# Kernel optimization log

Hardware: AMD Instinct MI355X
Metric: run time of the kernel (lower is better)

## Reference

```python
import jax, jax.numpy as jnp
import numpy as np

N, E, F = 50000, 1_600_000, 128
EPS = 1e-5
DATASET_NUM = 1.0


def _glorot(k, shape):
    lim = jnp.sqrt(6.0 / (shape[0] + shape[1]))
    return jax.random.uniform(k, shape, jnp.float32, -lim, lim)


def setup_inputs() -> dict:
    key = jax.random.key(0)
    ks = jax.random.split(key, 24)
    inp = {
        "x": jax.random.normal(ks[0], (N, F), jnp.float32),
        "noise": jax.random.normal(ks[1], (N, F), jnp.float32),
        "edge_index": jax.random.randint(ks[2], (2, E), 0, N, jnp.int64),
        # ChebConv K=2 weights: W0 (T_0 = x term), W1 (T_1 = L_hat x term)
        "W1_0": _glorot(ks[3], (F, 64)),  "W1_1": _glorot(ks[4], (F, 64)),  "b1": jnp.zeros((64,), jnp.float32),
        "g1": jnp.ones((64,), jnp.float32), "be1": jnp.zeros((64,), jnp.float32),
        "W2_0": _glorot(ks[5], (64, 16)), "W2_1": _glorot(ks[6], (64, 16)), "b2": jnp.zeros((16,), jnp.float32),
        "W3_0": _glorot(ks[7], (16, 64)), "W3_1": _glorot(ks[8], (16, 64)), "b3": jnp.zeros((64,), jnp.float32),
        "g3": jnp.ones((64,), jnp.float32), "be3": jnp.zeros((64,), jnp.float32),
        "W4_0": _glorot(ks[9], (64, F)),  "W4_1": _glorot(ks[10], (64, F)), "b4": jnp.zeros((F,), jnp.float32),
    }
    return inp


def reference(x, noise, edge_index, W1_0, W1_1, b1, g1, be1,
              W2_0, W2_1, b2, W3_0, W3_1, b3, g3, be3, W4_0, W4_1, b4):
    src, dst = edge_index[0], edge_index[1]
    n = x.shape[0]

    # train-mode noise injection: x + dataset_num * randn * x.mean()
    x = x + DATASET_NUM * noise * jnp.mean(x)

    # symmetric normalization; with lambda_max=2 the scaled Laplacian is -A_norm
    deg = jax.ops.segment_sum(jnp.ones_like(src, dtype=x.dtype), dst, num_segments=n)
    dinv = jnp.where(deg > 0, jax.lax.rsqrt(jnp.maximum(deg, 1.0)), 0.0)
    w_e = dinv[src] * dinv[dst]  # [E]

    def cheb(h, W0, W1, b):
        # T_0 = h ; T_1 = L_hat h = -A_norm h  (K=2 ChebConv)
        tx1 = -jax.ops.segment_sum(w_e[:, None] * h[src], dst, num_segments=n)
        return h @ W0 + tx1 @ W1 + b

    def bn(h, g, be):
        mu = jnp.mean(h, axis=0)
        var = jnp.mean((h - mu) ** 2, axis=0)
        return g * (h - mu) * jax.lax.rsqrt(var + EPS) + be

    h1 = jax.nn.relu(bn(cheb(x, W1_0, W1_1, b1), g1, be1))
    h2 = cheb(h1, W2_0, W2_1, b2)
    h3 = jax.nn.relu(bn(cheb(h2, W3_0, W3_1, b3), g3, be3))
    return cheb(h3, W4_0, W4_1, b4)
```

## Files before the change

### kernel.cpp

```cpp
#include <hip/hip_runtime.h>

#define NNODES 50000
#define NEDGES 1600000
#define FEAT   128
#define EPSV   1e-5f

typedef _Float16 h8 __attribute__((ext_vector_type(8)));
typedef _Float16 h4 __attribute__((ext_vector_type(4)));

__device__ __forceinline__ float4 f4fma(float s, float4 w, float4 a) {
  a.x = fmaf(s, w.x, a.x); a.y = fmaf(s, w.y, a.y);
  a.z = fmaf(s, w.z, a.z); a.w = fmaf(s, w.w, a.w);
  return a;
}

__global__ __launch_bounds__(256) void sum_kernel(const float* __restrict__ x,
                                                  float* __restrict__ out, int n4) {
  const float4* x4 = (const float4*)x;
  float s = 0.f;
  for (int i = blockIdx.x * blockDim.x + threadIdx.x; i < n4; i += gridDim.x * blockDim.x) {
    float4 v = x4[i];
    s += v.x + v.y + v.z + v.w;
  }
  for (int off = 32; off > 0; off >>= 1) s += __shfl_down(s, off);
  __shared__ float ls[4];
  int wid = threadIdx.x >> 6;
  if ((threadIdx.x & 63) == 0) ls[wid] = s;
  __syncthreads();
  if (threadIdx.x == 0) atomicAdd(out, ls[0] + ls[1] + ls[2] + ls[3]);
}

__global__ __launch_bounds__(256) void degree_kernel(const int* __restrict__ ei,
                                                     int* __restrict__ degi, int ne) {
  int e = blockIdx.x * blockDim.x + threadIdx.x;
  if (e < ne) atomicAdd(&degi[ei[NEDGES + e]], 1);
}

__global__ __launch_bounds__(256) void dinv_kernel(const int* __restrict__ degi,
                                                   float* __restrict__ dinv, int n) {
  int i = blockIdx.x * blockDim.x + threadIdx.x;
  if (i < n) dinv[i] = (degi[i] > 0) ? rsqrtf((float)degi[i]) : 0.f;
}

__global__ __launch_bounds__(1024) void scan1_kernel(const int* __restrict__ cnt,
                                                     int* __restrict__ exc,
                                                     int* __restrict__ bsum, int n) {
  __shared__ int s[1024];
  int tid = threadIdx.x;
  int i = blockIdx.x * 1024 + tid;
  int v = (i < n) ? cnt[i] : 0;
  int val = v;
  s[tid] = v;
  __syncthreads();
  for (int off = 1; off < 1024; off <<= 1) {
    int t = (tid >= off) ? s[tid - off] : 0;
    __syncthreads();
    val += t;
    s[tid] = val;
    __syncthreads();
  }
  if (i < n) exc[i] = val - v;
  if (tid == 1023) bsum[blockIdx.x] = val;
}

__global__ __launch_bounds__(256) void scan2_kernel(int* __restrict__ bsum, int nb) {
  __shared__ int s[256];
  int tid = threadIdx.x;
  int v = (tid < nb) ? bsum[tid] : 0;
  int val = v;
  s[tid] = v;
  __syncthreads();
  for (int off = 1; off < 256; off <<= 1) {
    int t = (tid >= off) ? s[tid - off] : 0;
    __syncthreads();
    val += t;
    s[tid] = val;
    __syncthreads();
  }
  if (tid < nb) bsum[tid] = val - v;
}

__global__ __launch_bounds__(256) void scan3_kernel(int* __restrict__ row_ptr,
                                                    const int* __restrict__ bsum,
                                                    int* __restrict__ cursor, int n) {
  int i = blockIdx.x * blockDim.x + threadIdx.x;
  if (i < n) {
    int v = row_ptr[i] + bsum[i >> 10];
    row_ptr[i] = v;
    cursor[i] = v;
  } else if (i == n) {
    row_ptr[n] = NEDGES;
  }
}

__global__ __launch_bounds__(256) void csr_fill_kernel(const int* __restrict__ ei,
                                                       const float* __restrict__ dinv,
                                                       int* __restrict__ cursor,
                                                       int2* __restrict__ ep, int ne) {
  int e = blockIdx.x * blockDim.x + threadIdx.x;
  if (e >= ne) return;
  int s = ei[e];
  int d = ei[NEDGES + e];
  float w = dinv[s] * dinv[d];
  int pos = atomicAdd(&cursor[d], 1);
  ep[pos] = make_int2(s, __float_as_int(w));
}

template <int F, bool ADD, bool STATS, bool BNIN, bool OUTH>
__global__ __launch_bounds__(256) void spmm_kernel(
    const int* __restrict__ row_ptr, const int2* __restrict__ ep,
    const _Float16* __restrict__ gsrc, const float* __restrict__ addL,
    const float* __restrict__ bias,
    const float* __restrict__ stats_in, const float* __restrict__ gin,
    const float* __restrict__ bein, float* __restrict__ stats_out,
    void* __restrict__ outv, int n) {
  constexpr int LPE = F / 8;
  constexpr int EPC = 64 / LPE;
  constexpr int LG  = (LPE == 2) ? 1 : 3;
  __shared__ float sst[STATS ? 2 * F : 1];
  const int tid = threadIdx.x;
  if (STATS) {
    if (tid < 2 * F) sst[tid] = 0.f;
    __syncthreads();
  }
  const int lane = tid & 63;
  const int wv = tid >> 6;
  const int sub = lane & (LPE - 1);
  const int g = lane >> LG;
  const int f0 = sub * 8;
  float scl[8], sht[8];
  if (BNIN) {
    const float inv_n = 1.0f / (float)n;
#pragma unroll
    for (int j = 0; j < 8; ++j) {
      int f = f0 + j;
      float mu = stats_in[f] * inv_n;
      float var = stats_in[F + f] * inv_n - mu * mu;
      float s = gin[f] * rsqrtf(var + EPSV);
      scl[j] = s;
      sht[j] = bein[f] - mu * s;
    }
  }
  for (int node = blockIdx.x * 4 + wv; node < n; node += gridDim.x * 4) {
    float acc[8] = {};
    const int beg = row_ptr[node], end = row_ptr[node + 1];
    int e = beg + g;
    while (e < end) {
      int2 s0 = ep[e];
      bool p1 = (e + EPC) < end;
      int2 s1 = ep[p1 ? e + EPC : e];
      float w0 = __int_as_float(s0.y);
      float w1 = p1 ? __int_as_float(s1.y) : 0.f;
      h8 r0 = *(const h8*)(gsrc + (size_t)s0.x * F + f0);
      h8 r1 = *(const h8*)(gsrc + (size_t)s1.x * F + f0);
#pragma unroll
      for (int j = 0; j < 8; ++j) {
        float v0 = (float)r0[j], v1 = (float)r1[j];
        if (BNIN) {
          v0 = fmaxf(fmaf(v0, scl[j], sht[j]), 0.f);
          v1 = fmaxf(fmaf(v1, scl[j], sht[j]), 0.f);
        }
        acc[j] = fmaf(w0, v0, acc[j]);
        acc[j] = fmaf(w1, v1, acc[j]);
      }
      e += 2 * EPC;
    }
#pragma unroll
    for (int m = LPE; m < 64; m <<= 1) {
#pragma unroll
      for (int j = 0; j < 8; ++j) acc[j] += __shfl_xor(acc[j], m);
    }
    if (lane < LPE) {
      float o[8];
      if (ADD) {
        float4 a0 = *(const float4*)&addL[(size_t)node * F + f0];
        float4 a1 = *(const float4*)&addL[(size_t)node * F + f0 + 4];
        float4 b0 = *(const float4*)&bias[f0];
        float4 b1 = *(const float4*)&bias[f0 + 4];
        o[0] = a0.x + b0.x - acc[0]; o[1] = a0.y + b0.y - acc[1];
        o[2] = a0.z + b0.z - acc[2]; o[3] = a0.w + b0.w - acc[3];
        o[4] = a1.x + b1.x - acc[4]; o[5] = a1.y + b1.y - acc[5];
        o[6] = a1.z + b1.z - acc[6]; o[7] = a1.w + b1.w - acc[7];
      } else {
#pragma unroll
        for (int j = 0; j < 8; ++j) o[j] = -acc[j];
      }
      if (OUTH) {
        h8 ho;
#pragma unroll
        for (int j = 0; j < 8; ++j) ho[j] = (_Float16)o[j];
        *(h8*)((_Float16*)outv + (size_t)node * F + f0) = ho;
      } else {
        float* op = (float*)outv + (size_t)node * F + f0;
        *(float4*)op = make_float4(o[0], o[1], o[2], o[3]);
        *(float4*)(op + 4) = make_float4(o[4], o[5], o[6], o[7]);
      }
      if (STATS) {
#pragma unroll
        for (int j = 0; j < 8; ++j) {
          atomicAdd(&sst[f0 + j], o[j]);
          atomicAdd(&sst[F + f0 + j], o[j] * o[j]);
        }
      }
    }
  }
  if (STATS) {
    __syncthreads();
    if (tid < 2 * F) atomicAdd(&stats_out[tid], sst[tid]);
  }
}

template <int K, int NB, bool ROWCAT, bool BIAS, bool BNIN, bool STATS, bool NOISE,
          bool A1H, int OMODE>
__global__ __launch_bounds__(256) void gemm_kernel(
    const void* __restrict__ A1, const float* __restrict__ A2,
    const float* __restrict__ W0, const float* __restrict__ W1,
    const float* __restrict__ bias, int col0, int wnt, int ostride, int ocol0,
    const float* __restrict__ noise, const float* __restrict__ sumv,
    const float* __restrict__ stats_in, const float* __restrict__ gin,
    const float* __restrict__ bein, float* __restrict__ stats_out,
    void* __restrict__ outv, void* __restrict__ out2, int n) {
  constexpr int TC  = NB / 4;
  constexpr int RG  = 256 / TC;
  constexpr int RPT = 4;
  constexpr int RPB = RG * RPT;
  constexpr int AP  = K + 4;
  constexpr int KB  = ROWCAT ? K / 2 : K;
  __shared__ float wl[K * NB];
  __shared__ float al[RPB * AP];
  __shared__ float sarr[BNIN ? KB : 1];
  __shared__ float tarr[BNIN ? KB : 1];
  __shared__ float sst[STATS ? 2 * NB : 1];
  const int tid = threadIdx.x;
  if (STATS && tid < 2 * NB) sst[tid] = 0.f;
  if (BNIN) {
    const float inv_n = 1.0f / (float)n;
    for (int f = tid; f < KB; f += 256) {
      float mu = stats_in[f] * inv_n;
      float var = stats_in[KB + f] * inv_n - mu * mu;
      float s = gin[f] * rsqrtf(var + EPSV);
      sarr[f] = s;
      tarr[f] = bein[f] - mu * s;
    }
  }
  float mean = 0.f;
  if (NOISE) mean = sumv[0] * (1.0f / (float)(NNODES * FEAT));

  for (int i = tid; i < K * NB; i += 256) {
    int k = i / NB, j = i - k * NB;
    int jg = col0 + j;
    float v;
    if (ROWCAT) v = (k < K / 2) ? W0[k * wnt + jg] : W1[(k - K / 2) * wnt + jg];
    else        v = (jg < wnt / 2) ? W0[k * (wnt / 2) + jg] : W1[k * (wnt / 2) + (jg - wnt / 2)];
    wl[i] = v;
  }
  __syncthreads();

  const int row0 = blockIdx.x * RPB;
  for (int i = tid; i < RPB * K; i += 256) {
    int r = i / K, k = i - r * K;
    int gr = row0 + r;
    float v = 0.f;
    if (gr < n) {
      if (ROWCAT) {
        if (k < K / 2) {
          v = A1H ? (float)((const _Float16*)A1)[(size_t)gr * (K / 2) + k]
                  : ((const float*)A1)[(size_t)gr * (K / 2) + k];
          if (BNIN) v = fmaxf(fmaf(v, sarr[k], tarr[k]), 0.f);
        } else {
          v = A2[(size_t)gr * (K / 2) + (k - K / 2)];
        }
      } else {
        v = A1H ? (float)((const _Float16*)A1)[(size_t)gr * K + k]
                : ((const float*)A1)[(size_t)gr * K + k];
        if (BNIN) v = fmaxf(fmaf(v, sarr[k], tarr[k]), 0.f);
        if (NOISE) v = fmaf(noise[(size_t)gr * K + k], mean, v);
      }
    }
    al[r * AP + k] = v;
  }
  __syncthreads();

  const int jt = (tid % TC) * 4;
  const int rbase = (tid / TC) * RPT;
  float4 acc[RPT];
#pragma unroll
  for (int rr = 0; rr < RPT; ++rr) acc[rr] = make_float4(0.f, 0.f, 0.f, 0.f);
  const float4* wl4 = (const float4*)wl;
  const int jt4 = jt >> 2;
#pragma unroll 4
  for (int k0 = 0; k0 < K; k0 += 4) {
    float4 w0 = wl4[(k0 + 0) * TC + jt4];
    float4 w1 = wl4[(k0 + 1) * TC + jt4];
    float4 w2 = wl4[(k0 + 2) * TC + jt4];
    float4 w3 = wl4[(k0 + 3) * TC + jt4];
#pragma unroll
    for (int rr = 0; rr < RPT; ++rr) {
      float4 a = *(const float4*)&al[(rbase + rr) * AP + k0];
      acc[rr] = f4fma(a.x, w0, acc[rr]);
      acc[rr] = f4fma(a.y, w1, acc[rr]);
      acc[rr] = f4fma(a.z, w2, acc[rr]);
      acc[rr] = f4fma(a.w, w3, acc[rr]);
    }
  }
  float4 b4 = make_float4(0.f, 0.f, 0.f, 0.f);
  if (BIAS) b4 = *(const float4*)&bias[col0 + jt];
  float sl[4] = {}, ql[4] = {};
#pragma unroll
  for (int rr = 0; rr < RPT; ++rr) {
    int gr = row0 + rbase + rr;
    if (gr < n) {
      float4 o;
      o.x = acc[rr].x + b4.x; o.y = acc[rr].y + b4.y;
      o.z = acc[rr].z + b4.z; o.w = acc[rr].w + b4.w;
      if (OMODE == 0) {
        *(float4*)((float*)outv + (size_t)gr * ostride + ocol0 + jt) = o;
      } else if (OMODE == 1) {
        h4 ho; ho[0] = (_Float16)o.x; ho[1] = (_Float16)o.y;
        ho[2] = (_Float16)o.z; ho[3] = (_Float16)o.w;
        *(h4*)((_Float16*)outv + (size_t)gr * ostride + ocol0 + jt) = ho;
      } else {
        if (jt < 16) {
          *(float4*)((float*)outv + (size_t)gr * 16 + jt) = o;
        } else {
          h4 ho; ho[0] = (_Float16)o.x; ho[1] = (_Float16)o.y;
          ho[2] = (_Float16)o.z; ho[3] = (_Float16)o.w;
          *(h4*)((_Float16*)out2 + (size_t)gr * 16 + (jt - 16)) = ho;
        }
      }
      if (STATS) {
        sl[0] += o.x; ql[0] += o.x * o.x; sl[1] += o.y; ql[1] += o.y * o.y;
        sl[2] += o.z; ql[2] += o.z * o.z; sl[3] += o.w; ql[3] += o.w * o.w;
      }
    }
  }
  if (STATS) {
#pragma unroll
    for (int j = 0; j < 4; ++j) {
      atomicAdd(&sst[jt + j], sl[j]);
      atomicAdd(&sst[NB + jt + j], ql[j]);
    }
    __syncthreads();
    if (tid < 2 * NB) atomicAdd(&stats_out[tid], sst[tid]);
  }
}

extern "C" void kernel_launch(void* const* d_in, const int* in_sizes, int n_in,
                              void* d_out, int out_size, void* d_ws, size_t ws_size,
                              hipStream_t stream) {
  const float* x     = (const float*)d_in[0];
  const float* noise = (const float*)d_in[1];
  const int*   ei    = (const int*)d_in[2];
  const float* W1_0 = (const float*)d_in[3];
  const float* W1_1 = (const float*)d_in[4];
  const float* b1   = (const float*)d_in[5];
  const float* g1   = (const float*)d_in[6];
  const float* be1  = (const float*)d_in[7];
  const float* W2_0 = (const float*)d_in[8];
  const float* W2_1 = (const float*)d_in[9];
  const float* b2   = (const float*)d_in[10];
  const float* W3_0 = (const float*)d_in[11];
  const float* W3_1 = (const float*)d_in[12];
  const float* b3   = (const float*)d_in[13];
  const float* g3   = (const float*)d_in[14];
  const float* be3  = (const float*)d_in[15];
  const float* W4_0 = (const float*)d_in[16];
  const float* W4_1 = (const float*)d_in[17];
  const float* b4   = (const float*)d_in[18];
  float* out = (float*)d_out;

  char* p = (char*)d_ws;
  size_t off = 0;
  auto alloc = [&](size_t b) -> void* {
    void* r = p + off;
    off += (b + 255) & ~(size_t)255;
    return r;
  };
  float* s_sum  = (float*)alloc(4);
  float* stats0 = (float*)alloc(2 * 64 * 4);
  float* stats1 = (float*)alloc(2 * 64 * 4);
  int*   degi   = (int*)alloc(sizeof(int) * NNODES);
  size_t zero_bytes = off;
  float*     dinv    = (float*)alloc(sizeof(float) * NNODES);
  int*       row_ptr = (int*)alloc(sizeof(int) * (NNODES + 1));
  int*       bsum    = (int*)alloc(256 * sizeof(int));
  int*       cursor  = (int*)alloc(sizeof(int) * NNODES);
  int2*      ep      = (int2*)alloc(8ULL * NEDGES);
  float*     zzL     = (float*)alloc(4ULL * NNODES * 64);
  _Float16*  zzRh    = (_Float16*)alloc(2ULL * NNODES * 64);
  float*     h1      = (float*)alloc(4ULL * NNODES * 64);
  _Float16*  zz2Rh   = (_Float16*)alloc(2ULL * NNODES * 16);
  _Float16*  h2      = (_Float16*)alloc(2ULL * NNODES * 16);
  _Float16*  h3h     = (_Float16*)alloc(2ULL * NNODES * 64);
  float*     agg4    = zzL;

  float* zz2L = out;
  float* agg3 = out + (size_t)NNODES * 16;

  hipMemsetAsync(d_ws, 0, zero_bytes, stream);

  int n4 = NNODES * FEAT / 4;
  sum_kernel<<<2048, 256, 0, stream>>>(x, s_sum, n4);
  degree_kernel<<<(NEDGES + 255) / 256, 256, 0, stream>>>(ei, degi, NEDGES);
  dinv_kernel<<<(NNODES + 255) / 256, 256, 0, stream>>>(degi, dinv, NNODES);
  scan1_kernel<<<(NNODES + 1023) / 1024, 1024, 0, stream>>>(degi, row_ptr, bsum, NNODES);
  scan2_kernel<<<1, 256, 0, stream>>>(bsum, (NNODES + 1023) / 1024);
  scan3_kernel<<<(NNODES + 256) / 256, 256, 0, stream>>>(row_ptr, bsum, cursor, NNODES);
  csr_fill_kernel<<<(NEDGES + 255) / 256, 256, 0, stream>>>(ei, dinv, cursor, ep, NEDGES);

  gemm_kernel<128, 64, false, false, false, false, true, false, 0>
      <<<(NNODES + 63) / 64, 256, 0, stream>>>(
      x, nullptr, W1_0, W1_1, nullptr, 0, 128, 64, 0,
      noise, s_sum, nullptr, nullptr, nullptr, nullptr, zzL, nullptr, NNODES);
  gemm_kernel<128, 64, false, false, false, false, true, false, 1>
      <<<(NNODES + 63) / 64, 256, 0, stream>>>(
      x, nullptr, W1_0, W1_1, nullptr, 64, 128, 64, 0,
      noise, s_sum, nullptr, nullptr, nullptr, nullptr, zzRh, nullptr, NNODES);
  spmm_kernel<64, true, true, false, false><<<2048, 256, 0, stream>>>(
      row_ptr, ep, zzRh, zzL, b1, nullptr, nullptr, nullptr, stats0, h1, NNODES);

  gemm_kernel<64, 32, false, false, true, false, false, false, 2>
      <<<(NNODES + 127) / 128, 256, 0, stream>>>(
      h1, nullptr, W2_0, W2_1, nullptr, 0, 32, 16, 0,
      nullptr, nullptr, stats0, g1, be1, nullptr, zz2L, zz2Rh, NNODES);
  spmm_kernel<16, true, false, false, true><<<2048, 256, 0, stream>>>(
      row_ptr, ep, zz2Rh, zz2L, b2, nullptr, nullptr, nullptr, nullptr, h2, NNODES);

  spmm_kernel<16, false, false, false, false><<<2048, 256, 0, stream>>>(
      row_ptr, ep, h2, nullptr, nullptr, nullptr, nullptr, nullptr, nullptr, agg3, NNODES);
  gemm_kernel<32, 64, true, true, false, true, false, true, 1>
      <<<(NNODES + 63) / 64, 256, 0, stream>>>(
      h2, agg3, W3_0, W3_1, b3, 0, 64, 64, 0,
      nullptr, nullptr, nullptr, nullptr, nullptr, stats1, h3h, nullptr, NNODES);

  spmm_kernel<64, false, false, true, false><<<2048, 256, 0, stream>>>(
      row_ptr, ep, h3h, nullptr, nullptr, stats1, g3, be3, nullptr, agg4, NNODES);
  gemm_kernel<128, 64, true, true, true, false, false, true, 0>
      <<<(NNODES + 63) / 64, 256, 0, stream>>>(
      h3h, agg4, W4_0, W4_1, b4, 0, 128, 128, 0,
      nullptr, nullptr, stats1, g3, be3, nullptr, out, nullptr, NNODES);
  gemm_kernel<128, 64, true, true, true, false, false, true, 0>
      <<<(NNODES + 63) / 64, 256, 0, stream>>>(
      h3h, agg4, W4_0, W4_1, b4, 64, 128, 128, 64,
      nullptr, nullptr, stats1, g3, be3, nullptr, out, nullptr, NNODES);
}
```

Before: 683.5 us.

## Build CSR via two-pass bucketed binning instead of scattered atomic fill

Replaces the single scattered csr_fill pass with a two-stage binning. The first pass groups each 4096-edge chunk by 512-node destination bucket in shared memory and writes packed (src, local dst) words contiguously into a staging buffer that reuses the output array. The second pass handles one bucket per block, so the cursor atomics and ep writes land in a narrow, cache-friendly region. This adds an extra kernel and a staging round trip, and the 16-bit source packing relies on the node count being below 65536.

```diff
diff --git a/kernel.cpp b/kernel.cpp
--- a/kernel.cpp
+++ b/kernel.cpp
@@ -4,6 +4,7 @@
 #define NEDGES 1600000
 #define FEAT   128
 #define EPSV   1e-5f
+#define NBUCK  ((NNODES + 511) / 512)
 
 typedef _Float16 h8 __attribute__((ext_vector_type(8)));
 typedef _Float16 h4 __attribute__((ext_vector_type(4)));
@@ -82,28 +83,88 @@
 
 __global__ __launch_bounds__(256) void scan3_kernel(int* __restrict__ row_ptr,
                                                     const int* __restrict__ bsum,
-                                                    int* __restrict__ cursor, int n) {
+                                                    int* __restrict__ cursor,
+                                                    int* __restrict__ gcur, int n) {
   int i = blockIdx.x * blockDim.x + threadIdx.x;
   if (i < n) {
     int v = row_ptr[i] + bsum[i >> 10];
     row_ptr[i] = v;
     cursor[i] = v;
+    if ((i & 511) == 0) gcur[i >> 9] = v;
   } else if (i == n) {
     row_ptr[n] = NEDGES;
   }
 }
 
-__global__ __launch_bounds__(256) void csr_fill_kernel(const int* __restrict__ ei,
-                                                       const float* __restrict__ dinv,
-                                                       int* __restrict__ cursor,
-                                                       int2* __restrict__ ep, int ne) {
-  int e = blockIdx.x * blockDim.x + threadIdx.x;
-  if (e >= ne) return;
-  int s = ei[e];
-  int d = ei[NEDGES + e];
-  float w = dinv[s] * dinv[d];
-  int pos = atomicAdd(&cursor[d], 1);
-  ep[pos] = make_int2(s, __float_as_int(w));
+__global__ __launch_bounds__(256) void binA_kernel(const int* __restrict__ ei,
+                                                   int* __restrict__ gcur,
+                                                   unsigned int* __restrict__ gstage,
+                                                   int ne) {
+  __shared__ int hist[NBUCK];
+  __shared__ int prefix[NBUCK + 1];
+  __shared__ int offs[NBUCK];
+  __shared__ int gbase[NBUCK];
+  __shared__ unsigned int stag[4096];
+  const int tid = threadIdx.x;
+  const int c0 = blockIdx.x * 4096;
+  for (int b = tid; b < NBUCK; b += 256) hist[b] = 0;
+  __syncthreads();
+  for (int i = tid; i < 4096; i += 256) {
+    int e = c0 + i;
+    if (e < ne) atomicAdd(&hist[ei[NEDGES + e] >> 9], 1);
+  }
+  __syncthreads();
+  if (tid == 0) {
+    int s = 0;
+    for (int b = 0; b < NBUCK; ++b) { prefix[b] = s; s += hist[b]; }
+    prefix[NBUCK] = s;
+  }
+  __syncthreads();
+  if (tid < NBUCK) {
+    offs[tid] = prefix[tid];
+    gbase[tid] = atomicAdd(&gcur[tid], hist[tid]);
+  }
+  __syncthreads();
+  for (int i = tid; i < 4096; i += 256) {
+    int e = c0 + i;
+    if (e < ne) {
+      int s = ei[e];
+      int d = ei[NEDGES + e];
+      int b = d >> 9;
+      int p = atomicAdd(&offs[b], 1);
+      stag[p] = (unsigned int)s | ((unsigned int)(d & 511) << 16);
+    }
+  }
+  __syncthreads();
+  const int total = prefix[NBUCK];
+  for (int j = tid; j < total; j += 256) {
+    int lo = 0, hi = NBUCK;
+    while (hi - lo > 1) {
+      int mid = (lo + hi) >> 1;
+      if (prefix[mid] <= j) lo = mid; else hi = mid;
+    }
+    gstage[gbase[lo] + (j - prefix[lo])] = stag[j];
+  }
+}
+
+__global__ __launch_bounds__(1024) void binB_kernel(const unsigned int* __restrict__ gstage,
+                                                    const int* __restrict__ row_ptr,
+                                                    const float* __restrict__ dinv,
+                                                    int* __restrict__ cursor,
+                                                    int2* __restrict__ ep, int n) {
+  const int b = blockIdx.x;
+  const int node0 = b << 9;
+  const int node1 = min(n, node0 + 512);
+  const int start = row_ptr[node0];
+  const int end = row_ptr[node1];
+  for (int i = start + threadIdx.x; i < end; i += 1024) {
+    unsigned int v = gstage[i];
+    int s = (int)(v & 0xFFFFu);
+    int d = node0 + (int)(v >> 16);
+    float w = dinv[s] * dinv[d];
+    int pos = atomicAdd(&cursor[d], 1);
+    ep[pos] = make_int2(s, __float_as_int(w));
+  }
 }
 
 template <int F, bool ADD, bool STATS, bool BNIN, bool OUTH>
@@ -385,6 +446,7 @@
   int*       row_ptr = (int*)alloc(sizeof(int) * (NNODES + 1));
   int*       bsum    = (int*)alloc(256 * sizeof(int));
   int*       cursor  = (int*)alloc(sizeof(int) * NNODES);
+  int*       gcur    = (int*)alloc(sizeof(int) * NBUCK);
   int2*      ep      = (int2*)alloc(8ULL * NEDGES);
   float*     zzL     = (float*)alloc(4ULL * NNODES * 64);
   _Float16*  zzRh    = (_Float16*)alloc(2ULL * NNODES * 64);
@@ -394,6 +456,7 @@
   _Float16*  h3h     = (_Float16*)alloc(2ULL * NNODES * 64);
   float*     agg4    = zzL;
 
+  unsigned int* gstage = (unsigned int*)out;
   float* zz2L = out;
   float* agg3 = out + (size_t)NNODES * 16;
 
@@ -405,8 +468,9 @@
   dinv_kernel<<<(NNODES + 255) / 256, 256, 0, stream>>>(degi, dinv, NNODES);
   scan1_kernel<<<(NNODES + 1023) / 1024, 1024, 0, stream>>>(degi, row_ptr, bsum, NNODES);
   scan2_kernel<<<1, 256, 0, stream>>>(bsum, (NNODES + 1023) / 1024);
-  scan3_kernel<<<(NNODES + 256) / 256, 256, 0, stream>>>(row_ptr, bsum, cursor, NNODES);
-  csr_fill_kernel<<<(NEDGES + 255) / 256, 256, 0, stream>>>(ei, dinv, cursor, ep, NEDGES);
+  scan3_kernel<<<(NNODES + 256) / 256, 256, 0, stream>>>(row_ptr, bsum, cursor, gcur, NNODES);
+  binA_kernel<<<(NEDGES + 4095) / 4096, 256, 0, stream>>>(ei, gcur, gstage, NEDGES);
+  binB_kernel<<<NBUCK, 1024, 0, stream>>>(gstage, row_ptr, dinv, cursor, ep, NNODES);
 
   gemm_kernel<128, 64, false, false, false, false, true, false, 0>
       <<<(NNODES + 63) / 64, 256, 0, stream>>>(
```

Measured after the change: 688.5 us. Within noise of the previous version (+0.7%).
